# Kernel optimization log

Measured on AMD Instinct MI355X. Metric: run time of the kernel, lower is better.

The kernel has to match this reference:

```python
import jax, jax.numpy as jnp
import numpy as np

B, S, H, K = 64, 512, 768, 21  # batch, seq_len, bert hidden, num_labels


def setup_inputs() -> dict:
    key = jax.random.key(0)
    ks = jax.random.split(key, 8)
    hidden = jax.random.normal(ks[0], (B, S, H), jnp.float32)  # post-BERT states
    W = jax.random.normal(ks[1], (H, K), jnp.float32) * 0.02    # classifier weight
    b = jnp.zeros((K,), jnp.float32)                            # classifier bias
    start_transitions = jax.random.uniform(ks[2], (K,), jnp.float32, -0.1, 0.1)
    transitions = jax.random.uniform(ks[3], (K, K), jnp.float32, -0.1, 0.1)
    end_transitions = jax.random.uniform(ks[4], (K,), jnp.float32, -0.1, 0.1)
    labels = jax.random.randint(ks[5], (B, S), 0, K)
    # torchcrf requires mask[:, 0] == 1; use variable-length prefix masks
    lengths = jax.random.randint(ks[6], (B,), S // 2, S + 1)
    attention_mask = jnp.arange(S)[None, :] < lengths[:, None]  # [B,S] bool
    return dict(hidden=hidden, W=W, b=b,
                start_transitions=start_transitions,
                transitions=transitions,
                end_transitions=end_transitions,
                labels=labels, attention_mask=attention_mask)


def _crf_nll(logits, labels, mask, start_t, trans, end_t):
    """torchcrf CRF forward (reduction='sum' log-likelihood), negated."""
    fmask = mask.astype(logits.dtype)  # [B,S]
    # ---- numerator: score of the gold path ----
    emit = jnp.take_along_axis(logits, labels[..., None], axis=2)[..., 0]  # [B,S]
    tr = trans[labels[:, :-1], labels[:, 1:]]                              # [B,S-1]
    num = start_t[labels[:, 0]] + emit[:, 0] \
        + jnp.sum((emit[:, 1:] + tr) * fmask[:, 1:], axis=1)
    lengths = mask.sum(axis=1)
    last_tags = jnp.take_along_axis(labels, (lengths - 1)[:, None], axis=1)[:, 0]
    num = num + end_t[last_tags]
    # ---- denominator: forward algorithm (logsumexp recurrence) ----
    alpha0 = start_t[None, :] + logits[:, 0]           # [B,K]
    ems = jnp.swapaxes(logits[:, 1:], 0, 1)            # [S-1,B,K]
    ms = jnp.swapaxes(mask[:, 1:], 0, 1)               # [S-1,B]

    def step(alpha, xs):
        em, m = xs
        nxt = jax.scipy.special.logsumexp(
            alpha[:, :, None] + trans[None, :, :] + em[:, None, :], axis=1)
        return jnp.where(m[:, None], nxt, alpha), None

    alpha, _ = jax.lax.scan(step, alpha0, (ems, ms))
    logZ = jax.scipy.special.logsumexp(alpha + end_t[None, :], axis=1)  # [B]
    return jnp.sum(logZ - num)  # negative log-likelihood (sum over batch)


def reference(hidden, W, b, start_transitions, transitions, end_transitions,
              labels, attention_mask):
    # dropout is identity in eval; the GRU in __init__ is unused in forward
    logits = hidden @ W + b  # [B,S,K]
    nll = _crf_nll(logits, labels, attention_mask,
                   start_transitions, transitions, end_transitions)
    # module returns (logits, -1 * log_likelihood) = (logits, nll)
    return (logits, nll)
```

## Files before the change

kernel.cpp:

```cpp
#include <hip/hip_runtime.h>

#define BSZ 64
#define SEQ 512
#define HID 768
#define NK  21

typedef short bf16x8 __attribute__((ext_vector_type(8)));
typedef float f32x4  __attribute__((ext_vector_type(4)));

__device__ __forceinline__ unsigned f2bf_pk(float lo, float hi) {
    unsigned ul = __float_as_uint(lo);
    unsigned uh = __float_as_uint(hi);
    ul = (ul + 0x7fffu + ((ul >> 16) & 1u)) >> 16;
    uh = (uh + 0x7fffu + ((uh >> 16) & 1u)) >> 16;
    return ul | (uh << 16);
}

#define WSTRIDE 784
__global__ __launch_bounds__(256) void gemm_bias_kernel(
    const float* __restrict__ hidden, const float* __restrict__ W,
    const float* __restrict__ bias, float* __restrict__ out)
{
    __shared__ unsigned short WlT[32 * WSTRIDE];

    const int tid  = threadIdx.x;
    const int lane = tid & 63;
    const int wv   = tid >> 6;
    const int n    = lane & 15;
    const int quad = lane >> 4;

    const int arow = blockIdx.x * 64 + wv * 16 + n;
    const float* ap = hidden + (size_t)arow * HID + quad * 8;

    float4 c0a = *(const float4*)(ap + 0);
    float4 c0b = *(const float4*)(ap + 4);

    for (int idx = tid; idx < HID * NK; idx += 256) {
        const int k = idx / NK;
        const int nn = idx - k * NK;
        const unsigned u = __float_as_uint(W[idx]);
        WlT[nn * WSTRIDE + k] =
            (unsigned short)((u + 0x7fffu + ((u >> 16) & 1u)) >> 16);
    }
    __syncthreads();

    const unsigned short* bp0 = WlT + n * WSTRIDE + quad * 8;
    const unsigned short* bp1 = WlT + (16 + n) * WSTRIDE + quad * 8;

    f32x4 acc0 = {0.f, 0.f, 0.f, 0.f};
    f32x4 acc1 = {0.f, 0.f, 0.f, 0.f};

    #pragma unroll
    for (int c = 0; c < HID / 32; ++c) {
        float4 c1a, c1b;
        if (c + 1 < HID / 32) {
            c1a = *(const float4*)(ap + (c + 1) * 32);
            c1b = *(const float4*)(ap + (c + 1) * 32 + 4);
        }
        union { bf16x8 v; unsigned u[4]; } af;
        af.u[0] = f2bf_pk(c0a.x, c0a.y);
        af.u[1] = f2bf_pk(c0a.z, c0a.w);
        af.u[2] = f2bf_pk(c0b.x, c0b.y);
        af.u[3] = f2bf_pk(c0b.z, c0b.w);

        const bf16x8 b0 = *(const bf16x8*)(bp0 + c * 32);
        const bf16x8 b1 = *(const bf16x8*)(bp1 + c * 32);

        acc0 = __builtin_amdgcn_mfma_f32_16x16x32_bf16(af.v, b0, acc0, 0, 0, 0);
        acc1 = __builtin_amdgcn_mfma_f32_16x16x32_bf16(af.v, b1, acc1, 0, 0, 0);
        c0a = c1a; c0b = c1b;
    }

    const float b0v = bias[n];
    const float b1v = (n < NK - 16) ? bias[16 + n] : 0.f;
    const int rbase = blockIdx.x * 64 + wv * 16 + quad * 4;
    #pragma unroll
    for (int r = 0; r < 4; ++r) {
        float* op = out + (size_t)(rbase + r) * NK;
        op[n] = acc0[r] + b0v;
        if (n < NK - 16) op[16 + n] = acc1[r] + b1v;
    }
}

__global__ __launch_bounds__(128) void crf_kernel(
    const float* __restrict__ logits,
    const float* __restrict__ start_t,
    const float* __restrict__ trans,
    const float* __restrict__ end_t,
    const int* __restrict__ labels,
    const int* __restrict__ mask,
    float* __restrict__ per_batch)
{
    __shared__ __align__(16) float Xl[SEQ * NK];
    __shared__ float C[SEQ];
    __shared__ float comb[24];

    const int b    = blockIdx.x;
    const int tid  = threadIdx.x;
    const int lane = tid & 63;
    const int wid  = tid >> 6;

    {
        const float4* g4 = (const float4*)(logits + (size_t)b * SEQ * NK);
        float4* l4 = (float4*)Xl;
        for (int idx = tid; idx < SEQ * NK / 4; idx += 128) l4[idx] = g4[idx];
    }

    const int* lab = labels + b * SEQ;
    const int* msk = mask   + b * SEQ;

    int cnt = 0;
    for (int t = lane; t < SEQ; t += 64) cnt += (msk[t] != 0);
    #pragma unroll
    for (int off = 32; off > 0; off >>= 1) cnt += __shfl_xor(cnt, off, 64);
    const int L = cnt;
    const int m = L >> 1;

    __syncthreads();

    {
        float numacc = 0.f;
        for (int t = tid; t < L; t += 128) {
            if (t == 0) numacc += start_t[lab[0]] + Xl[lab[0]];
            else        numacc += Xl[t * NK + lab[t]] + trans[lab[t - 1] * NK + lab[t]];
        }
        if (tid == 0) numacc += end_t[lab[L - 1]];
        #pragma unroll
        for (int off = 32; off > 0; off >>= 1) numacc += __shfl_xor(numacc, off, 64);
        if (lane == 0) comb[22 + wid] = numacc;
    }

    for (int t = tid; t < SEQ; t += 128) C[t] = Xl[t * NK];
    __syncthreads();

    for (int idx = tid; idx < SEQ * NK; idx += 128) {
        const int t = idx / NK;
        Xl[idx] = __expf(Xl[idx] - C[t]);
    }
    __syncthreads();

    const int jj = (lane < NK) ? lane : NK - 1;

#define RL(v, k) __uint_as_float(__builtin_amdgcn_readlane(__float_as_uint(v), k))
#define MATVEC(vv, EE, outv) do {                                          \
    float s0 = RL(vv, 0) * EE[0];                                          \
    float s1 = RL(vv, 1) * EE[1];                                          \
    float s2 = RL(vv, 2) * EE[2];                                          \
    s0 = fmaf(RL(vv,  3), EE[ 3], s0); s1 = fmaf(RL(vv,  4), EE[ 4], s1);  \
    s2 = fmaf(RL(vv,  5), EE[ 5], s2); s0 = fmaf(RL(vv,  6), EE[ 6], s0);  \
    s1 = fmaf(RL(vv,  7), EE[ 7], s1); s2 = fmaf(RL(vv,  8), EE[ 8], s2);  \
    s0 = fmaf(RL(vv,  9), EE[ 9], s0); s1 = fmaf(RL(vv, 10), EE[10], s1);  \
    s2 = fmaf(RL(vv, 11), EE[11], s2); s0 = fmaf(RL(vv, 12), EE[12], s0);  \
    s1 = fmaf(RL(vv, 13), EE[13], s1); s2 = fmaf(RL(vv, 14), EE[14], s2);  \
    s0 = fmaf(RL(vv, 15), EE[15], s0); s1 = fmaf(RL(vv, 16), EE[16], s1);  \
    s2 = fmaf(RL(vv, 17), EE[17], s2); s0 = fmaf(RL(vv, 18), EE[18], s0);  \
    s1 = fmaf(RL(vv, 19), EE[19], s1); s2 = fmaf(RL(vv, 20), EE[20], s2);  \
    outv = (s0 + s1) + s2;                                                 \
} while (0)
#define RENORM() do {                                                      \
    const float mm = __uint_as_float(                                      \
        __builtin_amdgcn_readfirstlane(__float_as_uint(a)));               \
    a *= __builtin_amdgcn_rcpf(mm);                                        \
    Orenorm += __logf(mm);                                                 \
} while (0)

    float a;
    float Orenorm = 0.f;
    float csum = 0.f;

    if (wid == 0) {
        float Ecol[NK];
        #pragma unroll
        for (int k = 0; k < NK; ++k) Ecol[k] = __expf(trans[k * NK + jj]);

        a = __expf(start_t[jj]) * Xl[jj];
        for (int t = lane; t <= m; t += 64) csum += C[t];

#define FSTEP(xr) do { float nv; MATVEC(a, Ecol, nv); a = nv * (xr); } while (0)
        int t0 = 1;
        for (; t0 + 7 <= m; t0 += 8) {
            const float* xb = Xl + t0 * NK + jj;
            const float x0 = xb[0];      const float x1 = xb[NK];
            const float x2 = xb[2 * NK]; const float x3 = xb[3 * NK];
            const float x4 = xb[4 * NK]; const float x5 = xb[5 * NK];
            const float x6 = xb[6 * NK]; const float x7 = xb[7 * NK];
            FSTEP(x0); FSTEP(x1); FSTEP(x2); FSTEP(x3);
            FSTEP(x4); FSTEP(x5); FSTEP(x6); FSTEP(x7);
            RENORM();
        }
        for (; t0 <= m; ++t0) { const float x = Xl[t0 * NK + jj]; FSTEP(x); }
#undef FSTEP
    } else {
        float Erow[NK];
        #pragma unroll
        for (int k = 0; k < NK; ++k) Erow[k] = __expf(trans[jj * NK + k]);

        a = __expf(end_t[jj]);
        for (int t = m + 1 + lane; t < L; t += 64) csum += C[t];

#define BSTEP(xr) do { const float u = a * (xr); float nv; MATVEC(u, Erow, nv); a = nv; } while (0)
        int t0 = L - 1;
        for (; t0 - 7 >= m + 1; t0 -= 8) {
            const float* xb = Xl + t0 * NK + jj;
            const float x0 = xb[0];       const float x1 = xb[-NK];
            const float x2 = xb[-2 * NK]; const float x3 = xb[-3 * NK];
            const float x4 = xb[-4 * NK]; const float x5 = xb[-5 * NK];
            const float x6 = xb[-6 * NK]; const float x7 = xb[-7 * NK];
            BSTEP(x0); BSTEP(x1); BSTEP(x2); BSTEP(x3);
            BSTEP(x4); BSTEP(x5); BSTEP(x6); BSTEP(x7);
            RENORM();
        }
        for (; t0 >= m + 1; --t0) { const float x = Xl[t0 * NK + jj]; BSTEP(x); }
#undef BSTEP
    }
#undef RL
#undef MATVEC
#undef RENORM

    #pragma unroll
    for (int off = 32; off > 0; off >>= 1) csum += __shfl_xor(csum, off, 64);

    if (wid == 1) {
        if (lane < NK) comb[lane] = a;
        if (lane == 0) comb[21] = csum + Orenorm;
    }
    __syncthreads();

    if (wid == 0) {
        float val = (lane < NK) ? a * comb[lane] : 0.f;
        #pragma unroll
        for (int off = 32; off > 0; off >>= 1) val += __shfl_xor(val, off, 64);
        if (lane == 0) {
            const float OF  = csum + Orenorm;
            const float num = comb[22] + comb[23];
            per_batch[b] = OF + comb[21] + __logf(val) - num;
        }
    }
}

__global__ __launch_bounds__(64) void reduce_kernel(
    const float* __restrict__ pb, float* __restrict__ out)
{
    float v = pb[threadIdx.x];
    #pragma unroll
    for (int off = 32; off > 0; off >>= 1) v += __shfl_xor(v, off, 64);
    if (threadIdx.x == 0) out[BSZ * SEQ * NK] = v;
}

extern "C" void kernel_launch(void* const* d_in, const int* in_sizes, int n_in,
                              void* d_out, int out_size, void* d_ws, size_t ws_size,
                              hipStream_t stream)
{
    const float* hidden  = (const float*)d_in[0];
    const float* W       = (const float*)d_in[1];
    const float* bias    = (const float*)d_in[2];
    const float* start_t = (const float*)d_in[3];
    const float* trans   = (const float*)d_in[4];
    const float* end_t   = (const float*)d_in[5];
    const int*   labels  = (const int*)d_in[6];
    const int*   mask    = (const int*)d_in[7];
    float* out = (float*)d_out;
    float* pb  = (float*)d_ws;

    gemm_bias_kernel<<<(BSZ * SEQ) / 64, 256, 0, stream>>>(hidden, W, bias, out);
    crf_kernel<<<BSZ, 128, 0, stream>>>(out, start_t, trans, end_t, labels, mask, pb);
    reduce_kernel<<<1, 64, 0, stream>>>(pb, out);
}
```

Measured before the change: 209.0 us.

## Pre-convert W to bf16 once and swap readlane for ds_bpermute in CRF matvec

A small kernel now transposes the classifier weight and converts it to bf16 once, so the GEMM reads B fragments straight from global/L2 instead of every block rebuilding a transposed shared-memory copy. That removes the per-block W staging loop, its integer division and the block-wide barrier, at the cost of one extra launch. Separately, the CRF matvec gathers alpha values across lanes with ds_bpermute instead of readlane, which changes the instruction mix on the serial recurrence.

Measured after the change: 208.3 us. No clear change (-0.3%).

```diff
diff --git a/kernel.cpp b/kernel.cpp
--- a/kernel.cpp
+++ b/kernel.cpp
@@ -8,21 +8,29 @@
 typedef short bf16x8 __attribute__((ext_vector_type(8)));
 typedef float f32x4  __attribute__((ext_vector_type(4)));
 
+__device__ __forceinline__ unsigned f2bf1(float x) {
+    unsigned u = __float_as_uint(x);
+    return (u + 0x7fffu + ((u >> 16) & 1u)) >> 16;
+}
 __device__ __forceinline__ unsigned f2bf_pk(float lo, float hi) {
-    unsigned ul = __float_as_uint(lo);
-    unsigned uh = __float_as_uint(hi);
-    ul = (ul + 0x7fffu + ((ul >> 16) & 1u)) >> 16;
-    uh = (uh + 0x7fffu + ((uh >> 16) & 1u)) >> 16;
-    return ul | (uh << 16);
-}
-
-#define WSTRIDE 784
+    return f2bf1(lo) | (f2bf1(hi) << 16);
+}
+
+__global__ __launch_bounds__(256) void wconv_kernel(
+    const float* __restrict__ W, unsigned short* __restrict__ WT)
+{
+    const int idx = blockIdx.x * 256 + threadIdx.x;
+    const int n = idx / HID;
+    const int k = idx - n * HID;
+    unsigned short v = 0;
+    if (n < NK) v = (unsigned short)f2bf1(W[(size_t)k * NK + n]);
+    WT[idx] = v;
+}
+
 __global__ __launch_bounds__(256) void gemm_bias_kernel(
-    const float* __restrict__ hidden, const float* __restrict__ W,
+    const float* __restrict__ hidden, const unsigned short* __restrict__ WT,
     const float* __restrict__ bias, float* __restrict__ out)
 {
-    __shared__ unsigned short WlT[32 * WSTRIDE];
-
     const int tid  = threadIdx.x;
     const int lane = tid & 63;
     const int wv   = tid >> 6;
@@ -31,24 +39,14 @@
 
     const int arow = blockIdx.x * 64 + wv * 16 + n;
     const float* ap = hidden + (size_t)arow * HID + quad * 8;
+    const bf16x8* bp0 = (const bf16x8*)(WT + (size_t)n * HID + quad * 8);
+    const bf16x8* bp1 = (const bf16x8*)(WT + (size_t)(16 + n) * HID + quad * 8);
+
+    f32x4 acc0 = {0.f, 0.f, 0.f, 0.f};
+    f32x4 acc1 = {0.f, 0.f, 0.f, 0.f};
 
     float4 c0a = *(const float4*)(ap + 0);
     float4 c0b = *(const float4*)(ap + 4);
-
-    for (int idx = tid; idx < HID * NK; idx += 256) {
-        const int k = idx / NK;
-        const int nn = idx - k * NK;
-        const unsigned u = __float_as_uint(W[idx]);
-        WlT[nn * WSTRIDE + k] =
-            (unsigned short)((u + 0x7fffu + ((u >> 16) & 1u)) >> 16);
-    }
-    __syncthreads();
-
-    const unsigned short* bp0 = WlT + n * WSTRIDE + quad * 8;
-    const unsigned short* bp1 = WlT + (16 + n) * WSTRIDE + quad * 8;
-
-    f32x4 acc0 = {0.f, 0.f, 0.f, 0.f};
-    f32x4 acc1 = {0.f, 0.f, 0.f, 0.f};
 
     #pragma unroll
     for (int c = 0; c < HID / 32; ++c) {
@@ -63,8 +61,8 @@
         af.u[2] = f2bf_pk(c0b.x, c0b.y);
         af.u[3] = f2bf_pk(c0b.z, c0b.w);
 
-        const bf16x8 b0 = *(const bf16x8*)(bp0 + c * 32);
-        const bf16x8 b1 = *(const bf16x8*)(bp1 + c * 32);
+        const bf16x8 b0 = bp0[c * 4];
+        const bf16x8 b1 = bp1[c * 4];
 
         acc0 = __builtin_amdgcn_mfma_f32_16x16x32_bf16(af.v, b0, acc0, 0, 0, 0);
         acc1 = __builtin_amdgcn_mfma_f32_16x16x32_bf16(af.v, b1, acc1, 0, 0, 0);
@@ -141,20 +139,20 @@
 
     const int jj = (lane < NK) ? lane : NK - 1;
 
-#define RL(v, k) __uint_as_float(__builtin_amdgcn_readlane(__float_as_uint(v), k))
+#define BP(v, k) __uint_as_float(__builtin_amdgcn_ds_bpermute(4 * (k), __float_as_uint(v)))
 #define MATVEC(vv, EE, outv) do {                                          \
-    float s0 = RL(vv, 0) * EE[0];                                          \
-    float s1 = RL(vv, 1) * EE[1];                                          \
-    float s2 = RL(vv, 2) * EE[2];                                          \
-    s0 = fmaf(RL(vv,  3), EE[ 3], s0); s1 = fmaf(RL(vv,  4), EE[ 4], s1);  \
-    s2 = fmaf(RL(vv,  5), EE[ 5], s2); s0 = fmaf(RL(vv,  6), EE[ 6], s0);  \
-    s1 = fmaf(RL(vv,  7), EE[ 7], s1); s2 = fmaf(RL(vv,  8), EE[ 8], s2);  \
-    s0 = fmaf(RL(vv,  9), EE[ 9], s0); s1 = fmaf(RL(vv, 10), EE[10], s1);  \
-    s2 = fmaf(RL(vv, 11), EE[11], s2); s0 = fmaf(RL(vv, 12), EE[12], s0);  \
-    s1 = fmaf(RL(vv, 13), EE[13], s1); s2 = fmaf(RL(vv, 14), EE[14], s2);  \
-    s0 = fmaf(RL(vv, 15), EE[15], s0); s1 = fmaf(RL(vv, 16), EE[16], s1);  \
-    s2 = fmaf(RL(vv, 17), EE[17], s2); s0 = fmaf(RL(vv, 18), EE[18], s0);  \
-    s1 = fmaf(RL(vv, 19), EE[19], s1); s2 = fmaf(RL(vv, 20), EE[20], s2);  \
+    float s0 = BP(vv, 0) * EE[0];                                          \
+    float s1 = BP(vv, 1) * EE[1];                                          \
+    float s2 = BP(vv, 2) * EE[2];                                          \
+    s0 = fmaf(BP(vv,  3), EE[ 3], s0); s1 = fmaf(BP(vv,  4), EE[ 4], s1);  \
+    s2 = fmaf(BP(vv,  5), EE[ 5], s2); s0 = fmaf(BP(vv,  6), EE[ 6], s0);  \
+    s1 = fmaf(BP(vv,  7), EE[ 7], s1); s2 = fmaf(BP(vv,  8), EE[ 8], s2);  \
+    s0 = fmaf(BP(vv,  9), EE[ 9], s0); s1 = fmaf(BP(vv, 10), EE[10], s1);  \
+    s2 = fmaf(BP(vv, 11), EE[11], s2); s0 = fmaf(BP(vv, 12), EE[12], s0);  \
+    s1 = fmaf(BP(vv, 13), EE[13], s1); s2 = fmaf(BP(vv, 14), EE[14], s2);  \
+    s0 = fmaf(BP(vv, 15), EE[15], s0); s1 = fmaf(BP(vv, 16), EE[16], s1);  \
+    s2 = fmaf(BP(vv, 17), EE[17], s2); s0 = fmaf(BP(vv, 18), EE[18], s0);  \
+    s1 = fmaf(BP(vv, 19), EE[19], s1); s2 = fmaf(BP(vv, 20), EE[20], s2);  \
     outv = (s0 + s1) + s2;                                                 \
 } while (0)
 #define RENORM() do {                                                      \
@@ -213,7 +211,7 @@
         for (; t0 >= m + 1; --t0) { const float x = Xl[t0 * NK + jj]; BSTEP(x); }
 #undef BSTEP
     }
-#undef RL
+#undef BP
 #undef MATVEC
 #undef RENORM
 
@@ -260,9 +258,12 @@
     const int*   labels  = (const int*)d_in[6];
     const int*   mask    = (const int*)d_in[7];
     float* out = (float*)d_out;
-    float* pb  = (float*)d_ws;
-
-    gemm_bias_kernel<<<(BSZ * SEQ) / 64, 256, 0, stream>>>(hidden, W, bias, out);
+
+    float*          pb = (float*)d_ws;
+    unsigned short* WT = (unsigned short*)((char*)d_ws + 256);
+
+    wconv_kernel<<<(32 * HID) / 256, 256, 0, stream>>>(W, WT);
+    gemm_bias_kernel<<<(BSZ * SEQ) / 64, 256, 0, stream>>>(hidden, WT, bias, out);
     crf_kernel<<<BSZ, 128, 0, stream>>>(out, start_t, trans, end_t, labels, mask, pb);
     reduce_kernel<<<1, 64, 0, stream>>>(pb, out);
 }
```
